# Optimization experiments

Measured on AMD Instinct MI355X. Metric: run time of the kernel, lower is better.

Reference implementation:

```python
import jax, jax.numpy as jnp
import numpy as np

B, S, D, E, H, TOP_K = 8, 2048, 512, 10, 2048, 2

def setup_inputs() -> dict:
    key = jax.random.key(0)
    ks = jax.random.split(key, 8)
    sd = 0.02
    return {
        "x": jax.random.normal(ks[0], (B, S, D), jnp.float32),
        "noise": jax.random.normal(ks[1], (B, S, E), jnp.float32),
        "Wr": jax.random.normal(ks[2], (D, E), jnp.float32) * sd,
        "br": jnp.zeros((E,), jnp.float32),
        "Wn": jax.random.normal(ks[3], (D, E), jnp.float32) * sd,
        "bn": jnp.zeros((E,), jnp.float32),
        "W1": jax.random.normal(ks[4], (E, D, H), jnp.float32) * sd,
        "b1": jnp.zeros((E, H), jnp.float32),
        "W2": jax.random.normal(ks[5], (E, H, D), jnp.float32) * sd,
        "b2": jnp.zeros((E, D), jnp.float32),
    }

def reference(x, noise, Wr, br, Wn, bn, W1, b1, W2, b2):
    # Noisy top-k router
    logits = x @ Wr + br                                  # [B,S,E]
    noise_logits = x @ Wn + bn                            # [B,S,E]
    noisy = logits + noise * jax.nn.softplus(noise_logits)
    top_vals, top_idx = jax.lax.top_k(noisy, TOP_K)       # [B,S,k]
    # softmax over -inf-scattered logits == softmax over top-k values scattered back
    g_topk = jax.nn.softmax(top_vals, axis=-1)            # [B,S,k]
    n_exp = Wr.shape[-1]
    gating = jnp.sum(jax.nn.one_hot(top_idx, n_exp, dtype=x.dtype) * g_topk[..., None], axis=-2)  # [B,S,E]
    # Dense combine: gating is exactly zero for unselected experts, so weighting
    # every expert's FFN output reproduces the masked gather/scatter loop.
    out = jnp.zeros_like(x)
    for e in range(n_exp):  # small fixed expert count
        h = jax.nn.relu(x @ W1[e] + b1[e])                # [B,S,H]
        y = h @ W2[e] + b2[e]                             # [B,S,D]
        out = out + gating[..., e:e+1] * y
    return out
```

## Files before the change

kernel.cpp:

```cpp
#include <hip/hip_runtime.h>
#include <hip/hip_bf16.h>
#include <stdint.h>


#define N_TOK 16384
#define DIM 512
#define NEXP 10
#define HID 2048
#define BM 128
#define BN 128
#define BK 64
#define MAXSLOT (2*N_TOK + NEXP*BM)
#define NMB (MAXSLOT/BM)
#define RT_TOK 32
#define NBN1 (HID/BN)
#define NBN2 (DIM/BN)

typedef __attribute__((ext_vector_type(8))) short bf16x8;
typedef __attribute__((ext_vector_type(4))) float f32x4;

__device__ __forceinline__ unsigned short f2bf(float v) {
  __hip_bfloat16 h = __float2bfloat16(v);
  return *reinterpret_cast<unsigned short*>(&h);
}

__device__ __forceinline__ float bf2f(unsigned short u) {
  union { unsigned int i; float f; } c;
  c.i = ((unsigned int)u) << 16;
  return c.f;
}

__device__ __forceinline__ void gload_lds16(const void* g, void* l) {
  __builtin_amdgcn_global_load_lds(
      (__attribute__((address_space(1))) void*)g,
      (__attribute__((address_space(3))) void*)l, 16, 0, 0);
}

__device__ __forceinline__ int xcd_chunk(int b, int nwg) {
  int q = nwg >> 3, r = nwg & 7;
  int xcd = b & 7, slot = b >> 3;
  return (xcd < r) ? (xcd*(q+1) + slot) : (r*(q+1) + (xcd-r)*q + slot);
}

__global__ void k_cvt_x(const float* __restrict__ x, unsigned short* __restrict__ xb) {
  size_t i = (size_t)blockIdx.x * 256 + threadIdx.x;
  const float4* xp = (const float4*)x;
  float4 a = xp[2*i], b = xp[2*i+1];
  union { unsigned short us[8]; uint4 u4; } p;
  p.us[0]=f2bf(a.x); p.us[1]=f2bf(a.y); p.us[2]=f2bf(a.z); p.us[3]=f2bf(a.w);
  p.us[4]=f2bf(b.x); p.us[5]=f2bf(b.y); p.us[6]=f2bf(b.z); p.us[7]=f2bf(b.w);
  ((uint4*)xb)[i] = p.u4;
}

__global__ void k_cvt_router_w(const float* __restrict__ Wr, const float* __restrict__ Wn,
                               float* __restrict__ wrt, float* __restrict__ wnt) {
  int i = blockIdx.x * 256 + threadIdx.x;
  if (i < NEXP*DIM) {
    int e = i / DIM, d = i % DIM;
    wrt[i] = Wr[d*NEXP + e];
    wnt[i] = Wn[d*NEXP + e];
  }
}

__global__ void k_transpose(const float* __restrict__ in, unsigned short* __restrict__ outp,
                            int R, int C) {
  __shared__ float tile[64][65];
  int nTR = R >> 6, nTC = C >> 6;
  int b = blockIdx.x;
  int tilesPerE = nTR * nTC;
  int e = b / tilesPerE;
  int t = b % tilesPerE;
  int rb = t / nTC, cb = t % nTC;
  int tr = threadIdx.x >> 6, tc = threadIdx.x & 63;
  const float* ip = in + ((size_t)e*R + (size_t)rb*64) * C + cb*64;
  #pragma unroll
  for (int p = 0; p < 16; ++p)
    tile[p*4 + tr][tc] = ip[(size_t)(p*4 + tr)*C + tc];
  __syncthreads();
  unsigned short* op = outp + ((size_t)e*C + (size_t)cb*64) * R + rb*64;
  int ro = threadIdx.x >> 2;
  int cc = (threadIdx.x & 3) * 16;
  union { unsigned short us[8]; bf16x8 v; } pk;
  #pragma unroll
  for (int half = 0; half < 2; ++half) {
    #pragma unroll
    for (int j = 0; j < 8; ++j) pk.us[j] = f2bf(tile[cc + half*8 + j][ro]);
    *(bf16x8*)&op[(size_t)ro*R + cc + half*8] = pk.v;
  }
}

__global__ __launch_bounds__(256) void k_router2(
    const float* __restrict__ x, const float* __restrict__ noise,
    const float* __restrict__ wrt, const float* __restrict__ wnt,
    const float* __restrict__ br, const float* __restrict__ bnb,
    int* __restrict__ top_idx, float* __restrict__ top_gate, int* __restrict__ counts) {
  __shared__ float part[8][RT_TOK][21];
  __shared__ float red[RT_TOK][21];
  __shared__ float vsh[RT_TOK][10];
  __shared__ int lcnt[16];
  int tid = threadIdx.x;
  int tl = tid & 31;
  int g  = tid >> 5;
  int tok = blockIdx.x * RT_TOK + tl;

  const float4* xr = (const float4*)(x + (size_t)tok*DIM + g*64);
  float acc[20];
  #pragma unroll
  for (int j = 0; j < 20; ++j) acc[j] = 0.f;

  #pragma unroll 4
  for (int c = 0; c < 16; ++c) {
    float4 xv = xr[c];
    int d = g*64 + c*4;
    #pragma unroll
    for (int e = 0; e < NEXP; ++e) {
      float4 a = *(const float4*)(wrt + e*DIM + d);
      float4 b = *(const float4*)(wnt + e*DIM + d);
      acc[e]      += xv.x*a.x + xv.y*a.y + xv.z*a.z + xv.w*a.w;
      acc[10+e]   += xv.x*b.x + xv.y*b.y + xv.z*b.z + xv.w*b.w;
    }
  }
  #pragma unroll
  for (int j = 0; j < 20; ++j) part[g][tl][j] = acc[j];
  __syncthreads();

  for (int o = tid; o < RT_TOK*20; o += 256) {
    int t2 = o / 20, j = o % 20;
    float s = 0.f;
    #pragma unroll
    for (int gg = 0; gg < 8; ++gg) s += part[gg][t2][j];
    red[t2][j] = s;
  }
  __syncthreads();

  for (int o = tid; o < RT_TOK*NEXP; o += 256) {
    int t2 = o / NEXP, e = o % NEXP;
    float nl = red[t2][10+e] + bnb[e];
    float sp = (nl > 20.f) ? nl : log1pf(expf(nl));
    vsh[t2][e] = red[t2][e] + br[e]
               + noise[(size_t)(blockIdx.x*RT_TOK + t2)*NEXP + e] * sp;
  }
  if (tid < 16) lcnt[tid] = 0;
  __syncthreads();

  if (tid < RT_TOK) {
    int t2 = tid;
    float v0 = -1e30f, v1 = -1e30f; int i0 = 0, i1 = 0;
    #pragma unroll
    for (int e = 0; e < NEXP; ++e) {
      float v = vsh[t2][e];
      if (v > v0) { v1 = v0; i1 = i0; v0 = v; i0 = e; }
      else if (v > v1) { v1 = v; i1 = e; }
    }
    float ev = expf(v1 - v0);
    float g0 = 1.f / (1.f + ev);
    float g1 = ev / (1.f + ev);
    int tk = blockIdx.x * RT_TOK + t2;
    top_idx[tk*2] = i0; top_idx[tk*2+1] = i1;
    top_gate[tk*2] = g0; top_gate[tk*2+1] = g1;
    atomicAdd(&lcnt[i0], 1);
    atomicAdd(&lcnt[i1], 1);
  }
  __syncthreads();
  if (tid < NEXP && lcnt[tid] > 0) atomicAdd(&counts[tid], lcnt[tid]);
}

__global__ void k_offsets(const int* __restrict__ counts, int* __restrict__ cursors,
                          int* __restrict__ offs) {
  if (threadIdx.x == 0 && blockIdx.x == 0) {
    int acc = 0;
    for (int e = 0; e < NEXP; ++e) {
      offs[e] = acc; cursors[e] = acc;
      acc += ((counts[e] + BM - 1) / BM) * BM;
    }
    offs[NEXP] = acc;
  }
}

__global__ __launch_bounds__(256) void k_scatter(
    const int* __restrict__ top_idx,
    int* __restrict__ cursors, int* __restrict__ slot_token,
    int* __restrict__ tok_slot) {
  __shared__ int lcnt[16];
  __shared__ int lbase[16];
  int tid = threadIdx.x;
  int t = blockIdx.x * 256 + tid;
  if (tid < 16) lcnt[tid] = 0;
  __syncthreads();
  int e0 = top_idx[t*2], e1 = top_idx[t*2+1];
  int r0 = atomicAdd(&lcnt[e0], 1);
  int r1 = atomicAdd(&lcnt[e1], 1);
  __syncthreads();
  if (tid < NEXP && lcnt[tid] > 0) lbase[tid] = atomicAdd(&cursors[tid], lcnt[tid]);
  __syncthreads();
  int p0 = lbase[e0] + r0;
  int p1 = lbase[e1] + r1;
  slot_token[p0] = t;
  slot_token[p1] = t;
  tok_slot[t*2]   = p0;
  tok_slot[t*2+1] = p1;
}

__global__ __launch_bounds__(256, 4) void k_gemm1(
    const unsigned short* __restrict__ xb, const unsigned short* __restrict__ w1t,
    const float* __restrict__ b1, const int* __restrict__ slot_token,
    const int* __restrict__ offs, unsigned short* __restrict__ h) {
  __shared__ unsigned short smem[2*BM*BK];
  unsigned short* As = smem;
  unsigned short* Bs = smem + BM*BK;
  int w = xcd_chunk(blockIdx.x, NMB*NBN1);
  int bm = w / NBN1, bn = w % NBN1;
  int tid = threadIdx.x, wid = tid >> 6, lane = tid & 63;
  int s0 = bm * BM;
  int e = 0;
  #pragma unroll
  for (int i = 1; i < NEXP; ++i) if (s0 >= offs[i]) e = i;

  int tokA[4];
  #pragma unroll
  for (int i = 0; i < 4; ++i) {
    int r = (i*4 + wid)*8 + (lane >> 3);
    int t = slot_token[s0 + r];
    tokA[i] = t < 0 ? 0 : t;
  }
  int kcs = ((lane & 7) ^ (lane >> 3)) * 8;
  int ldst = (lane & 7) * 8;
  const unsigned short* w1te = w1t + ((size_t)e*HID + (size_t)bn*BN) * DIM;

  f32x4 acc[4][4];
  #pragma unroll
  for (int m=0;m<4;m++)
    #pragma unroll
    for (int n=0;n<4;n++) acc[m][n] = (f32x4){0.f,0.f,0.f,0.f};

  int wr = wid >> 1, wc = wid & 1;
  int xr = (lane & 7) * 8;

  for (int kt = 0; kt < DIM/BK; ++kt) {
    int k0 = kt * BK;
    #pragma unroll
    for (int i = 0; i < 4; ++i) {
      int r = (i*4 + wid)*8 + (lane >> 3);
      gload_lds16(xb + (size_t)tokA[i]*DIM + k0 + kcs, &As[r*BK + ldst]);
      gload_lds16(w1te + (size_t)r*DIM + k0 + kcs, &Bs[r*BK + ldst]);
    }
    __syncthreads();
    #pragma unroll
    for (int ks = 0; ks < 2; ++ks) {
      int kk = (ks*32 + (lane >> 4)*8) ^ xr;
      bf16x8 a[4], b[4];
      #pragma unroll
      for (int m=0;m<4;m++) a[m] = *(const bf16x8*)&As[(wr*64 + m*16 + (lane&15))*BK + kk];
      #pragma unroll
      for (int n=0;n<4;n++) b[n] = *(const bf16x8*)&Bs[(wc*64 + n*16 + (lane&15))*BK + kk];
      #pragma unroll
      for (int m=0;m<4;m++)
        #pragma unroll
        for (int n=0;n<4;n++)
          acc[m][n] = __builtin_amdgcn_mfma_f32_16x16x32_bf16(a[m], b[n], acc[m][n], 0,0,0);
    }
    __syncthreads();
  }

  unsigned short* ct = smem;
  #pragma unroll
  for (int m=0;m<4;m++){
    int row0 = wr*64 + m*16 + (lane>>4)*4;
    #pragma unroll
    for (int n=0;n<4;n++){
      int lcol = wc*64 + n*16 + (lane&15);
      float bias = b1[e*HID + bn*BN + lcol];
      #pragma unroll
      for (int r=0;r<4;r++){
        int row = row0 + r;
        float v = acc[m][n][r] + bias;
        v = v > 0.f ? v : 0.f;
        int pc = (lcol >> 3) ^ (row & 7);
        ct[row*BN + (pc<<3) + (lcol&7)] = f2bf(v);
      }
    }
  }
  __syncthreads();
  int cchunk = tid & 15, rbase = tid >> 4;
  unsigned short* hb = h + (size_t)s0*HID + bn*BN;
  #pragma unroll
  for (int j=0;j<8;j++){
    int row = rbase + j*16;
    int pc = cchunk ^ (row & 7);
    bf16x8 v = *(const bf16x8*)&ct[row*BN + (pc<<3)];
    *(bf16x8*)&hb[(size_t)row*HID + cchunk*8] = v;
  }
}

__global__ __launch_bounds__(256, 4) void k_gemm2(
    const unsigned short* __restrict__ h, const unsigned short* __restrict__ w2t,
    const float* __restrict__ b2, const int* __restrict__ offs,
    unsigned short* __restrict__ ybuf) {
  __shared__ unsigned short smem[2*BM*BK];
  unsigned short* As = smem;
  unsigned short* Bs = smem + BM*BK;
  int w = xcd_chunk(blockIdx.x, NMB*NBN2);
  int bm = w / NBN2, bn = w % NBN2;
  int tid = threadIdx.x, wid = tid >> 6, lane = tid & 63;
  int s0 = bm * BM;
  int e = 0;
  #pragma unroll
  for (int i = 1; i < NEXP; ++i) if (s0 >= offs[i]) e = i;
  int kcs = ((lane & 7) ^ (lane >> 3)) * 8;
  int ldst = (lane & 7) * 8;
  const unsigned short* w2te = w2t + ((size_t)e*DIM + (size_t)bn*BN) * HID;

  f32x4 acc[4][4];
  #pragma unroll
  for (int m=0;m<4;m++)
    #pragma unroll
    for (int n=0;n<4;n++) acc[m][n] = (f32x4){0.f,0.f,0.f,0.f};

  int wr = wid >> 1, wc = wid & 1;
  int xr = (lane & 7) * 8;

  for (int kt = 0; kt < HID/BK; ++kt) {
    int k0 = kt * BK;
    #pragma unroll
    for (int i = 0; i < 4; ++i) {
      int r = (i*4 + wid)*8 + (lane >> 3);
      gload_lds16(h + (size_t)(s0 + r)*HID + k0 + kcs, &As[r*BK + ldst]);
      gload_lds16(w2te + (size_t)r*HID + k0 + kcs, &Bs[r*BK + ldst]);
    }
    __syncthreads();
    #pragma unroll
    for (int ks = 0; ks < 2; ++ks) {
      int kk = (ks*32 + (lane >> 4)*8) ^ xr;
      bf16x8 a[4], b[4];
      #pragma unroll
      for (int m=0;m<4;m++) a[m] = *(const bf16x8*)&As[(wr*64 + m*16 + (lane&15))*BK + kk];
      #pragma unroll
      for (int n=0;n<4;n++) b[n] = *(const bf16x8*)&Bs[(wc*64 + n*16 + (lane&15))*BK + kk];
      #pragma unroll
      for (int m=0;m<4;m++)
        #pragma unroll
        for (int n=0;n<4;n++)
          acc[m][n] = __builtin_amdgcn_mfma_f32_16x16x32_bf16(a[m], b[n], acc[m][n], 0,0,0);
    }
    __syncthreads();
  }

  unsigned short* ct = smem;
  #pragma unroll
  for (int m=0;m<4;m++){
    int row0 = wr*64 + m*16 + (lane>>4)*4;
    #pragma unroll
    for (int n=0;n<4;n++){
      int lcol = wc*64 + n*16 + (lane&15);
      float bias = b2[e*DIM + bn*BN + lcol];
      #pragma unroll
      for (int r=0;r<4;r++){
        int row = row0 + r;
        int pc = (lcol >> 3) ^ (row & 7);
        ct[row*BN + (pc<<3) + (lcol&7)] = f2bf(acc[m][n][r] + bias);
      }
    }
  }
  __syncthreads();
  int cchunk = tid & 15, rbase = tid >> 4;
  unsigned short* yb = ybuf + (size_t)s0*DIM + bn*BN;
  #pragma unroll
  for (int j=0;j<8;j++){
    int row = rbase + j*16;
    int pc = cchunk ^ (row & 7);
    bf16x8 v = *(const bf16x8*)&ct[row*BN + (pc<<3)];
    *(bf16x8*)&yb[(size_t)row*DIM + cchunk*8] = v;
  }
}

__global__ __launch_bounds__(256) void k_combine(
    const unsigned short* __restrict__ ybuf, const int* __restrict__ tok_slot,
    const float* __restrict__ top_gate, float* __restrict__ out) {
  int gid = blockIdx.x * 256 + threadIdx.x;
  int t = gid >> 6, j = (gid & 63) * 8;
  int s0 = tok_slot[t*2], s1 = tok_slot[t*2+1];
  float g0 = top_gate[t*2], g1 = top_gate[t*2+1];
  union { bf16x8 v; unsigned short us[8]; } y0, y1;
  y0.v = *(const bf16x8*)&ybuf[(size_t)s0*DIM + j];
  y1.v = *(const bf16x8*)&ybuf[(size_t)s1*DIM + j];
  float4 o0, o1;
  float* op0 = &o0.x;
  float* op1 = &o1.x;
  #pragma unroll
  for (int i = 0; i < 4; ++i) op0[i] = g0*bf2f(y0.us[i])   + g1*bf2f(y1.us[i]);
  #pragma unroll
  for (int i = 0; i < 4; ++i) op1[i] = g0*bf2f(y0.us[4+i]) + g1*bf2f(y1.us[4+i]);
  float4* dst = (float4*)&out[(size_t)t*DIM + j];
  dst[0] = o0; dst[1] = o1;
}

extern "C" void kernel_launch(void* const* d_in, const int* in_sizes, int n_in,
                              void* d_out, int out_size, void* d_ws, size_t ws_size,
                              hipStream_t stream) {
  const float* x   = (const float*)d_in[0];
  const float* noi = (const float*)d_in[1];
  const float* Wr  = (const float*)d_in[2];
  const float* br  = (const float*)d_in[3];
  const float* Wn  = (const float*)d_in[4];
  const float* bnb = (const float*)d_in[5];
  const float* W1  = (const float*)d_in[6];
  const float* b1  = (const float*)d_in[7];
  const float* W2  = (const float*)d_in[8];
  const float* b2  = (const float*)d_in[9];
  float* out = (float*)d_out;
  (void)in_sizes; (void)n_in; (void)ws_size; (void)out_size;

  char* ws = (char*)d_ws;
  size_t off = 0;
  auto alloc = [&](size_t bytes) -> void* {
    void* p = ws + off; off += (bytes + 255) & ~(size_t)255; return p;
  };
  unsigned short* w1t  = (unsigned short*)alloc((size_t)NEXP*HID*DIM*2);
  unsigned short* xb   = (unsigned short*)alloc((size_t)N_TOK*DIM*2);
  unsigned short* w2t  = (unsigned short*)alloc((size_t)NEXP*DIM*HID*2);
  unsigned short* hbuf = (unsigned short*)alloc((size_t)MAXSLOT*HID*2);
  float* wrt = (float*)alloc(NEXP*DIM*4);
  float* wnt = (float*)alloc(NEXP*DIM*4);
  int*   top_idx  = (int*)alloc(N_TOK*2*4);
  float* top_gate = (float*)alloc(N_TOK*2*4);
  int*   slot_token = (int*)alloc((size_t)MAXSLOT*4);
  int*   tok_slot   = (int*)alloc((size_t)N_TOK*2*4);
  int*   ctrl = (int*)alloc(64*4);
  int* counts  = ctrl;
  int* cursors = ctrl + 10;
  int* offs    = ctrl + 20;
  unsigned short* ybuf = w1t;

  hipMemsetAsync(ctrl, 0, 64*4, stream);
  hipMemsetAsync(slot_token, 0xFF, (size_t)MAXSLOT*4, stream);

  k_cvt_x<<<(N_TOK*DIM/8)/256, 256, 0, stream>>>(x, xb);
  k_cvt_router_w<<<(NEXP*DIM+255)/256, 256, 0, stream>>>(Wr, Wn, wrt, wnt);
  k_transpose<<<NEXP*(DIM/64)*(HID/64), 256, 0, stream>>>(W1, w1t, DIM, HID);
  k_transpose<<<NEXP*(HID/64)*(DIM/64), 256, 0, stream>>>(W2, w2t, HID, DIM);
  k_router2<<<N_TOK/RT_TOK, 256, 0, stream>>>(x, noi, wrt, wnt, br, bnb, top_idx, top_gate, counts);
  k_offsets<<<1, 64, 0, stream>>>(counts, cursors, offs);
  k_scatter<<<N_TOK/256, 256, 0, stream>>>(top_idx, cursors, slot_token, tok_slot);
  k_gemm1<<<NMB*NBN1, 256, 0, stream>>>(xb, w1t, b1, slot_token, offs, hbuf);
  k_gemm2<<<NMB*NBN2, 256, 0, stream>>>(hbuf, w2t, b2, offs, ybuf);
  k_combine<<<(N_TOK*64)/256, 256, 0, stream>>>(ybuf, tok_slot, top_gate, out);
}
```

Baseline: 269.4 us.

## Fuse prep kernels, fold x conversion into router, merge offsets into scatter

Merges the W1/W2 transposes and router-weight transpose into one launch, and folds the fp32-to-bf16 conversion of x into the router kernel, which already reads x. The offsets computation is folded into the scatter kernel: each block recomputes the per-expert offsets locally from counts, cursors now hold relative positions, and block 0 writes the global offsets. This removes four kernel launches and a second full read of x, at the cost of redundant offset computation per block and extra stores in the router.

New measurement: 268.0 us, median of 2. Within noise of the previous version (-0.5%).

```diff
diff --git a/kernel.cpp b/kernel.cpp
--- a/kernel.cpp
+++ b/kernel.cpp
@@ -42,32 +42,12 @@
   return (xcd < r) ? (xcd*(q+1) + slot) : (r*(q+1) + (xcd-r)*q + slot);
 }
 
-__global__ void k_cvt_x(const float* __restrict__ x, unsigned short* __restrict__ xb) {
-  size_t i = (size_t)blockIdx.x * 256 + threadIdx.x;
-  const float4* xp = (const float4*)x;
-  float4 a = xp[2*i], b = xp[2*i+1];
-  union { unsigned short us[8]; uint4 u4; } p;
-  p.us[0]=f2bf(a.x); p.us[1]=f2bf(a.y); p.us[2]=f2bf(a.z); p.us[3]=f2bf(a.w);
-  p.us[4]=f2bf(b.x); p.us[5]=f2bf(b.y); p.us[6]=f2bf(b.z); p.us[7]=f2bf(b.w);
-  ((uint4*)xb)[i] = p.u4;
-}
-
-__global__ void k_cvt_router_w(const float* __restrict__ Wr, const float* __restrict__ Wn,
-                               float* __restrict__ wrt, float* __restrict__ wnt) {
-  int i = blockIdx.x * 256 + threadIdx.x;
-  if (i < NEXP*DIM) {
-    int e = i / DIM, d = i % DIM;
-    wrt[i] = Wr[d*NEXP + e];
-    wnt[i] = Wn[d*NEXP + e];
-  }
-}
-
-__global__ void k_transpose(const float* __restrict__ in, unsigned short* __restrict__ outp,
-                            int R, int C) {
+__device__ __forceinline__ void transpose_tile(
+    const float* __restrict__ in, unsigned short* __restrict__ outp,
+    int R, int C, int b) {
   __shared__ float tile[64][65];
-  int nTR = R >> 6, nTC = C >> 6;
-  int b = blockIdx.x;
-  int tilesPerE = nTR * nTC;
+  int nTC = C >> 6;
+  int tilesPerE = (R >> 6) * nTC;
   int e = b / tilesPerE;
   int t = b % tilesPerE;
   int rb = t / nTC, cb = t % nTC;
@@ -89,11 +69,33 @@
   }
 }
 
-__global__ __launch_bounds__(256) void k_router2(
+#define NT_W1 (NEXP*(DIM/64)*(HID/64))
+#define NT_W2 (NEXP*(HID/64)*(DIM/64))
+
+__global__ void k_prep(const float* __restrict__ W1, unsigned short* __restrict__ w1t,
+                       const float* __restrict__ W2, unsigned short* __restrict__ w2t,
+                       const float* __restrict__ Wr, const float* __restrict__ Wn,
+                       float* __restrict__ wrt, float* __restrict__ wnt) {
+  int b = blockIdx.x;
+  if (b < NT_W1) {
+    transpose_tile(W1, w1t, DIM, HID, b);
+  } else if (b < NT_W1 + NT_W2) {
+    transpose_tile(W2, w2t, HID, DIM, b - NT_W1);
+  } else {
+    for (int i = threadIdx.x; i < NEXP*DIM; i += 256) {
+      int e = i / DIM, d = i % DIM;
+      wrt[i] = Wr[d*NEXP + e];
+      wnt[i] = Wn[d*NEXP + e];
+    }
+  }
+}
+
+__global__ __launch_bounds__(256) void k_router2x(
     const float* __restrict__ x, const float* __restrict__ noise,
     const float* __restrict__ wrt, const float* __restrict__ wnt,
     const float* __restrict__ br, const float* __restrict__ bnb,
-    int* __restrict__ top_idx, float* __restrict__ top_gate, int* __restrict__ counts) {
+    int* __restrict__ top_idx, float* __restrict__ top_gate, int* __restrict__ counts,
+    unsigned short* __restrict__ xb) {
   __shared__ float part[8][RT_TOK][21];
   __shared__ float red[RT_TOK][21];
   __shared__ float vsh[RT_TOK][10];
@@ -108,6 +110,7 @@
   #pragma unroll
   for (int j = 0; j < 20; ++j) acc[j] = 0.f;
 
+  float4 xprev;
   #pragma unroll 4
   for (int c = 0; c < 16; ++c) {
     float4 xv = xr[c];
@@ -118,6 +121,14 @@
       float4 b = *(const float4*)(wnt + e*DIM + d);
       acc[e]      += xv.x*a.x + xv.y*a.y + xv.z*a.z + xv.w*a.w;
       acc[10+e]   += xv.x*b.x + xv.y*b.y + xv.z*b.z + xv.w*b.w;
+    }
+    if (c & 1) {
+      union { unsigned short us[8]; uint4 u4; } p;
+      p.us[0]=f2bf(xprev.x); p.us[1]=f2bf(xprev.y); p.us[2]=f2bf(xprev.z); p.us[3]=f2bf(xprev.w);
+      p.us[4]=f2bf(xv.x);    p.us[5]=f2bf(xv.y);    p.us[6]=f2bf(xv.z);    p.us[7]=f2bf(xv.w);
+      *(uint4*)&xb[(size_t)tok*DIM + g*64 + (c-1)*4] = p.u4;
+    } else {
+      xprev = xv;
     }
   }
   #pragma unroll
@@ -165,27 +176,25 @@
   if (tid < NEXP && lcnt[tid] > 0) atomicAdd(&counts[tid], lcnt[tid]);
 }
 
-__global__ void k_offsets(const int* __restrict__ counts, int* __restrict__ cursors,
-                          int* __restrict__ offs) {
-  if (threadIdx.x == 0 && blockIdx.x == 0) {
-    int acc = 0;
-    for (int e = 0; e < NEXP; ++e) {
-      offs[e] = acc; cursors[e] = acc;
-      acc += ((counts[e] + BM - 1) / BM) * BM;
-    }
-    offs[NEXP] = acc;
-  }
-}
-
-__global__ __launch_bounds__(256) void k_scatter(
-    const int* __restrict__ top_idx,
-    int* __restrict__ cursors, int* __restrict__ slot_token,
-    int* __restrict__ tok_slot) {
+__global__ __launch_bounds__(256) void k_scatter2(
+    const int* __restrict__ top_idx, const int* __restrict__ counts,
+    int* __restrict__ cursors, int* __restrict__ offs_g,
+    int* __restrict__ slot_token, int* __restrict__ tok_slot) {
   __shared__ int lcnt[16];
   __shared__ int lbase[16];
+  __shared__ int loffs[12];
   int tid = threadIdx.x;
   int t = blockIdx.x * 256 + tid;
   if (tid < 16) lcnt[tid] = 0;
+  if (tid == 0) {
+    int acc = 0;
+    #pragma unroll
+    for (int e = 0; e < NEXP; ++e) {
+      loffs[e] = acc;
+      acc += ((counts[e] + BM - 1) / BM) * BM;
+    }
+    loffs[NEXP] = acc;
+  }
   __syncthreads();
   int e0 = top_idx[t*2], e1 = top_idx[t*2+1];
   int r0 = atomicAdd(&lcnt[e0], 1);
@@ -193,12 +202,13 @@
   __syncthreads();
   if (tid < NEXP && lcnt[tid] > 0) lbase[tid] = atomicAdd(&cursors[tid], lcnt[tid]);
   __syncthreads();
-  int p0 = lbase[e0] + r0;
-  int p1 = lbase[e1] + r1;
+  int p0 = loffs[e0] + lbase[e0] + r0;
+  int p1 = loffs[e1] + lbase[e1] + r1;
   slot_token[p0] = t;
   slot_token[p1] = t;
   tok_slot[t*2]   = p0;
   tok_slot[t*2+1] = p1;
+  if (blockIdx.x == 0 && tid <= NEXP) offs_g[tid] = loffs[tid];
 }
 
 __global__ __launch_bounds__(256, 4) void k_gemm1(
@@ -434,13 +444,11 @@
   hipMemsetAsync(ctrl, 0, 64*4, stream);
   hipMemsetAsync(slot_token, 0xFF, (size_t)MAXSLOT*4, stream);
 
-  k_cvt_x<<<(N_TOK*DIM/8)/256, 256, 0, stream>>>(x, xb);
-  k_cvt_router_w<<<(NEXP*DIM+255)/256, 256, 0, stream>>>(Wr, Wn, wrt, wnt);
-  k_transpose<<<NEXP*(DIM/64)*(HID/64), 256, 0, stream>>>(W1, w1t, DIM, HID);
-  k_transpose<<<NEXP*(HID/64)*(DIM/64), 256, 0, stream>>>(W2, w2t, HID, DIM);
-  k_router2<<<N_TOK/RT_TOK, 256, 0, stream>>>(x, noi, wrt, wnt, br, bnb, top_idx, top_gate, counts);
-  k_offsets<<<1, 64, 0, stream>>>(counts, cursors, offs);
-  k_scatter<<<N_TOK/256, 256, 0, stream>>>(top_idx, cursors, slot_token, tok_slot);
+  k_prep<<<NT_W1 + NT_W2 + 1, 256, 0, stream>>>(W1, w1t, W2, w2t, Wr, Wn, wrt, wnt);
+  k_router2x<<<N_TOK/RT_TOK, 256, 0, stream>>>(x, noi, wrt, wnt, br, bnb,
+                                               top_idx, top_gate, counts, xb);
+  k_scatter2<<<N_TOK/256, 256, 0, stream>>>(top_idx, counts, cursors, offs,
+                                            slot_token, tok_slot);
   k_gemm1<<<NMB*NBN1, 256, 0, stream>>>(xb, w1t, b1, slot_token, offs, hbuf);
   k_gemm2<<<NMB*NBN2, 256, 0, stream>>>(hbuf, w2t, b2, offs, ybuf);
   k_combine<<<(N_TOK*64)/256, 256, 0, stream>>>(ybuf, tok_slot, top_gate, out);
```
